# Kernel tuning notes

Measured on AMD Instinct MI355X. Metric: run time of the kernel, lower is better.

Reference implementation:

```python
import jax, jax.numpy as jnp
import numpy as np

EPS = 1e-12  # numerical guard for sqrt (matches the 1e-12 used in the module's p3 path)


def _chamfer_p3(p, q):
    # p, q: (2, B, N, 4) complex 4-momenta (channel 0 = real, 1 = imag)
    p3 = p[..., 1:]  # (2, B, N, 3) spatial 3-momenta
    q3 = q[..., 1:]  # (2, B, M, 3)
    # pairwise euclidean distance via ||p||^2 + ||q||^2 - 2 p.q (cdist, p=2),
    # batched independently over the complex channel and batch dims.
    p_sq = jnp.sum(p3 * p3, axis=-1)  # (2, B, N)
    q_sq = jnp.sum(q3 * q3, axis=-1)  # (2, B, M)
    cross = jnp.einsum('cbnd,cbmd->cbnm', p3, q3)  # (2, B, N, M)
    d2 = p_sq[..., :, None] + q_sq[..., None, :] - 2.0 * cross
    dist = jnp.sqrt(jnp.maximum(d2, 0.0) + EPS)  # (2, B, N, M)
    min_pq = jnp.min(dist, axis=-1)  # (2, B, N)
    min_qp = jnp.min(dist, axis=-2)  # (2, B, M)
    return jnp.sum(min_pq) + jnp.sum(min_qp)


def setup_inputs() -> dict:
    key = jax.random.key(0)
    k1, k2 = jax.random.split(key)
    B, N, M = 64, 1024, 1024
    p = jax.random.normal(k1, (2, B, N, 4), dtype=jnp.float32)
    q = jax.random.normal(k2, (2, B, M, 4), dtype=jnp.float32)
    return {"p": p, "q": q}


def reference(p, q):
    return _chamfer_p3(p, q)
```

## Files before the change

kernel.cpp:

```cpp
#include <hip/hip_runtime.h>


typedef short bf16x8 __attribute__((ext_vector_type(8)));
typedef float f32x16 __attribute__((ext_vector_type(16)));

#define ONE_BF 0x3f80

__device__ __forceinline__ unsigned short f2bf(float x) {
    unsigned u = __float_as_uint(x);
    u += 0x7fffu + ((u >> 16) & 1u);
    return (unsigned short)(u >> 16);
}
__device__ __forceinline__ float bf2f(unsigned short h) {
    return __uint_as_float(((unsigned)h) << 16);
}

__global__ __launch_bounds__(256, 2) void chamfer_dir(
    const float4* __restrict__ P, const float4* __restrict__ Q,
    float* __restrict__ out)
{
    __shared__ short lAh[1024 * 8];
    __shared__ short lAl[1024 * 8];
    __shared__ short lB[512 * 16];
    __shared__ float wsum[4];

    const int blk   = blockIdx.x;
    const int batch = blk >> 2;
    const int dir   = (blk >> 1) & 1;
    const int cb    = blk & 1;
    const int t     = threadIdx.x;
    const int base  = batch << 10;

    const float4* __restrict__ ownb = (dir ? Q : P) + base;
    const float4* __restrict__ oppb = (dir ? P : Q) + base;

#pragma unroll
    for (int i = 0; i < 4; ++i) {
        const int pt = t + (i << 8);
        float4 v = ownb[pt];
        float psq = v.y * v.y + v.z * v.z + v.w * v.w;
        unsigned short psqh = f2bf(psq);
        unsigned short psql = f2bf(psq - bf2f(psqh));
        unsigned short yh = f2bf(v.y), zh = f2bf(v.z), wh = f2bf(v.w);
        unsigned short m2yh = f2bf(-2.0f * bf2f(yh));
        unsigned short m2zh = f2bf(-2.0f * bf2f(zh));
        unsigned short m2wh = f2bf(-2.0f * bf2f(wh));
        unsigned short m2yl = f2bf(-2.0f * (v.y - bf2f(yh)));
        unsigned short m2zl = f2bf(-2.0f * (v.z - bf2f(zh)));
        unsigned short m2wl = f2bf(-2.0f * (v.w - bf2f(wh)));
        bf16x8 ah = { (short)psqh, (short)psql, (short)m2yh, (short)m2zh,
                      (short)m2wh, (short)m2yl, (short)m2zl, (short)m2wl };
        bf16x8 al = { (short)m2yh, (short)m2zh, (short)m2wh,
                      (short)ONE_BF, (short)ONE_BF, 0, 0, 0 };
        *(bf16x8*)&lAh[pt * 8] = ah;
        *(bf16x8*)&lAl[pt * 8] = al;
    }
#pragma unroll
    for (int i = 0; i < 2; ++i) {
        const int pt = t + (i << 8);
        float4 v = oppb[(cb << 9) + pt];
        float qsq = v.y * v.y + v.z * v.z + v.w * v.w;
        unsigned short qsqh = f2bf(qsq);
        unsigned short qsql = f2bf(qsq - bf2f(qsqh));
        unsigned short yh = f2bf(v.y), zh = f2bf(v.z), wh = f2bf(v.w);
        unsigned short yl = f2bf(v.y - bf2f(yh));
        unsigned short zl = f2bf(v.z - bf2f(zh));
        unsigned short wl = f2bf(v.w - bf2f(wh));
        bf16x8 bh = { (short)ONE_BF, (short)ONE_BF, (short)yh, (short)zh,
                      (short)wh, (short)yh, (short)zh, (short)wh };
        bf16x8 bl = { (short)yl, (short)zl, (short)wl,
                      (short)qsqh, (short)qsql, 0, 0, 0 };
        *(bf16x8*)&lB[pt * 16]     = bh;
        *(bf16x8*)&lB[pt * 16 + 8] = bl;
    }
    __syncthreads();

    const int lane = t & 63;
    const int half = lane >> 5;
    const int l31  = lane & 31;
    const int wv   = t >> 6;

    const short* aptr = half ? lAl : lAh;

    bf16x8 bf[4];
#pragma unroll
    for (int k = 0; k < 4; ++k) {
        const int pt = ((wv << 2) + k) * 32 + l31;
        bf[k] = *(const bf16x8*)&lB[(pt * 2 + half) * 8];
    }

    f32x16 zf;
#pragma unroll
    for (int j = 0; j < 16; ++j) zf[j] = 0.0f;

    f32x16 acc[4];
#pragma unroll
    for (int k = 0; k < 4; ++k)
#pragma unroll
        for (int j = 0; j < 16; ++j) acc[k][j] = 3.4e38f;

    for (int rt = 0; rt < 32; rt += 2) {
        bf16x8 af0 = *(const bf16x8*)&aptr[((rt << 5) + l31) * 8];
        bf16x8 af1 = *(const bf16x8*)&aptr[(((rt + 1) << 5) + l31) * 8];
#pragma unroll
        for (int k = 0; k < 4; ++k) {
            f32x16 ca = __builtin_amdgcn_mfma_f32_32x32x16_bf16(af0, bf[k], zf, 0, 0, 0);
            f32x16 cb2 = __builtin_amdgcn_mfma_f32_32x32x16_bf16(af1, bf[k], zf, 0, 0, 0);
#pragma unroll
            for (int j = 0; j < 16; ++j)
                acc[k][j] = fminf(fminf(ca[j], cb2[j]), acc[k][j]);
        }
    }

    float s = 0.0f;
#pragma unroll
    for (int k = 0; k < 4; ++k) {
        float m = acc[k][0];
#pragma unroll
        for (int j = 1; j < 16; ++j) m = fminf(m, acc[k][j]);
        m = fminf(m, __shfl_xor(m, 32, 64));
        if (half == 0) s += sqrtf(fmaxf(m, 0.0f) + 1e-12f);
    }
#pragma unroll
    for (int off = 32; off; off >>= 1) s += __shfl_down(s, off, 64);
    if (lane == 0) wsum[wv] = s;
    __syncthreads();
    if (t == 0) atomicAdd(out, wsum[0] + wsum[1] + wsum[2] + wsum[3]);
}

extern "C" void kernel_launch(void* const* d_in, const int* in_sizes, int n_in,
                              void* d_out, int out_size, void* d_ws, size_t ws_size,
                              hipStream_t stream) {
    const float4* P = (const float4*)d_in[0];
    const float4* Q = (const float4*)d_in[1];
    float* out = (float*)d_out;

    hipMemsetAsync(d_out, 0, sizeof(float), stream);
    chamfer_dir<<<dim3(128 * 2 * 2), dim3(256), 0, stream>>>(P, Q, out);
}
```

Baseline: 70.49 us.

## Split row range across two blocks and reduce partial minima in second kernel

```diff
diff --git a/kernel.cpp b/kernel.cpp
--- a/kernel.cpp
+++ b/kernel.cpp
@@ -15,19 +15,19 @@
     return __uint_as_float(((unsigned)h) << 16);
 }
 
-__global__ __launch_bounds__(256, 2) void chamfer_dir(
+__global__ __launch_bounds__(256, 4) void chamfer_main(
     const float4* __restrict__ P, const float4* __restrict__ Q,
-    float* __restrict__ out)
+    float* __restrict__ part)
 {
-    __shared__ short lAh[1024 * 8];
-    __shared__ short lAl[1024 * 8];
+    __shared__ short lAh[512 * 8];
+    __shared__ short lAl[512 * 8];
     __shared__ short lB[512 * 16];
-    __shared__ float wsum[4];
 
     const int blk   = blockIdx.x;
-    const int batch = blk >> 2;
-    const int dir   = (blk >> 1) & 1;
-    const int cb    = blk & 1;
+    const int batch = blk >> 3;
+    const int dir   = (blk >> 2) & 1;
+    const int cb    = (blk >> 1) & 1;
+    const int rb    = blk & 1;
     const int t     = threadIdx.x;
     const int base  = batch << 10;
 
@@ -35,9 +35,9 @@
     const float4* __restrict__ oppb = (dir ? P : Q) + base;
 
 #pragma unroll
-    for (int i = 0; i < 4; ++i) {
+    for (int i = 0; i < 2; ++i) {
         const int pt = t + (i << 8);
-        float4 v = ownb[pt];
+        float4 v = ownb[(rb << 9) + pt];
         float psq = v.y * v.y + v.z * v.z + v.w * v.w;
         unsigned short psqh = f2bf(psq);
         unsigned short psql = f2bf(psq - bf2f(psqh));
@@ -99,7 +99,7 @@
 #pragma unroll
         for (int j = 0; j < 16; ++j) acc[k][j] = 3.4e38f;
 
-    for (int rt = 0; rt < 32; rt += 2) {
+    for (int rt = 0; rt < 16; rt += 2) {
         bf16x8 af0 = *(const bf16x8*)&aptr[((rt << 5) + l31) * 8];
         bf16x8 af1 = *(const bf16x8*)&aptr[(((rt + 1) << 5) + l31) * 8];
 #pragma unroll
@@ -112,20 +112,36 @@
         }
     }
 
-    float s = 0.0f;
 #pragma unroll
     for (int k = 0; k < 4; ++k) {
         float m = acc[k][0];
 #pragma unroll
         for (int j = 1; j < 16; ++j) m = fminf(m, acc[k][j]);
         m = fminf(m, __shfl_xor(m, 32, 64));
-        if (half == 0) s += sqrtf(fmaxf(m, 0.0f) + 1e-12f);
+        if (half == 0) {
+            const int gcol = (cb << 9) + ((wv << 2) + k) * 32 + l31;
+            const int p = (((dir << 7) + batch) << 10) + gcol;
+            part[p * 2 + rb] = m;
+        }
+    }
+}
+
+__global__ __launch_bounds__(256) void chamfer_final(
+    const float2* __restrict__ part, float* __restrict__ out)
+{
+    __shared__ float ws[4];
+    const int t = threadIdx.x;
+    float s = 0.0f;
+    for (int i = blockIdx.x * 256 + t; i < (1 << 18); i += 128 * 256) {
+        float2 v = part[i];
+        float m = fminf(v.x, v.y);
+        s += sqrtf(fmaxf(m, 0.0f) + 1e-12f);
     }
 #pragma unroll
     for (int off = 32; off; off >>= 1) s += __shfl_down(s, off, 64);
-    if (lane == 0) wsum[wv] = s;
+    if ((t & 63) == 0) ws[t >> 6] = s;
     __syncthreads();
-    if (t == 0) atomicAdd(out, wsum[0] + wsum[1] + wsum[2] + wsum[3]);
+    if (t == 0) atomicAdd(out, ws[0] + ws[1] + ws[2] + ws[3]);
 }
 
 extern "C" void kernel_launch(void* const* d_in, const int* in_sizes, int n_in,
@@ -133,8 +149,10 @@
                               hipStream_t stream) {
     const float4* P = (const float4*)d_in[0];
     const float4* Q = (const float4*)d_in[1];
-    float* out = (float*)d_out;
+    float* out  = (float*)d_out;
+    float* part = (float*)d_ws;
 
     hipMemsetAsync(d_out, 0, sizeof(float), stream);
-    chamfer_dir<<<dim3(128 * 2 * 2), dim3(256), 0, stream>>>(P, Q, out);
+    chamfer_main<<<dim3(128 * 2 * 2 * 2), dim3(256), 0, stream>>>(P, Q, part);
+    chamfer_final<<<dim3(128), dim3(256), 0, stream>>>((const float2*)part, out);
 }
```

After: 81.60 us. 1.16x slower.
